# Optimization experiments

Hardware: AMD Instinct MI355X
Metric: run time of the kernel (lower is better)

## Reference

```python
import jax, jax.numpy as jnp
import numpy as np
import math

IN_DIM = 2048
OUT_DIM = 1152
SEQ_LEN = 8
WAY = 5
SHOT = 5
N_QUERIES = 100
MAX_LEN = int(SEQ_LEN * 1.5)
PE_SCALE = 0.1


def make_pe():
    pe = np.zeros((MAX_LEN, IN_DIM), dtype=np.float32)
    position = np.arange(0, MAX_LEN)[:, None].astype(np.float32)
    div_term = np.exp(np.arange(0, IN_DIM, 2).astype(np.float32) * -(math.log(10000.0) / IN_DIM))
    pe[:, 0::2] = np.sin(position * div_term) * PE_SCALE
    pe[:, 1::2] = np.cos(position * div_term) * PE_SCALE
    return jnp.asarray(pe)


def setup_inputs() -> dict:
    key = jax.random.key(0)
    ks = jax.random.split(key, 12)
    support_set = jax.random.normal(ks[0], (WAY * SHOT, SEQ_LEN, IN_DIM), dtype=jnp.float32)
    queries = jax.random.normal(ks[1], (N_QUERIES, SEQ_LEN, IN_DIM), dtype=jnp.float32)
    # labels: each class 0..WAY-1 appears SHOT times (sorted)
    support_labels = jnp.sort(jnp.arange(WAY * SHOT) % WAY)
    s = 1.0 / math.sqrt(IN_DIM)
    def lin(k):
        kw, kb = jax.random.split(k)
        W = jax.random.uniform(kw, (OUT_DIM, IN_DIM), minval=-s, maxval=s, dtype=jnp.float32)
        b = jax.random.uniform(kb, (OUT_DIM,), minval=-s, maxval=s, dtype=jnp.float32)
        return W, b
    sk_W, sk_b = lin(ks[2])
    sv_W, sv_b = lin(ks[3])
    qk_W, qk_b = lin(ks[4])
    qv_W, qv_b = lin(ks[5])
    return {
        "support_set": support_set,
        "support_labels": support_labels,
        "queries": queries,
        "sk_W": sk_W, "sk_b": sk_b,
        "sv_W": sv_W, "sv_b": sv_b,
        "qk_W": qk_W, "qk_b": qk_b,
        "qv_W": qv_W, "qv_b": qv_b,
        "ln_k_g": jnp.ones((OUT_DIM,), jnp.float32),
        "ln_k_b": jnp.zeros((OUT_DIM,), jnp.float32),
        "pe_table": make_pe(),
    }


def layer_norm(x, g, b, eps=1e-5):
    mu = jnp.mean(x, axis=-1, keepdims=True)
    var = jnp.var(x, axis=-1, keepdims=True)
    return (x - mu) / jnp.sqrt(var + eps) * g + b


def reference(support_set, support_labels, queries, sk_W, sk_b, sv_W, sv_b,
              qk_W, qk_b, qv_W, qv_b, ln_k_g, ln_k_b, pe_table):
    n_q, L, _ = queries.shape
    support_set = support_set + pe_table[None, :L]
    queries = queries + pe_table[None, :L]

    s_ks = layer_norm(support_set @ sk_W.T + sk_b, ln_k_g, ln_k_b)  # [S, L, D]
    q_ks = layer_norm(queries @ qk_W.T + qk_b, ln_k_g, ln_k_b)      # [Q, L, D]
    s_vs = support_set @ sv_W.T + sv_b                               # [S, L, D]
    q_vs = queries @ qv_W.T + qv_b                                   # [Q, L, D]

    D = q_ks.shape[-1]
    # group support by class: labels are sorted with equal shots per class
    k_bs = support_set.shape[0] // WAY
    class_k = s_ks.reshape(WAY, k_bs, L, D)   # [C, k, L, D]
    class_v = s_vs.reshape(WAY, k_bs, L, D)

    # scores: [C, Q, L(query), k*L(support)]
    scores = jnp.einsum('qld,ckmd->cqlkm', q_ks, class_k) / math.sqrt(D)
    scores = scores.reshape(WAY, n_q, L, k_bs * L)
    attn = jax.nn.softmax(scores, axis=-1)  # softmax over support frames per query frame
    attn = attn.reshape(WAY, n_q, L, k_bs, L).transpose(0, 1, 3, 2, 4)  # [C,Q,k,L,L]
    proto = jnp.einsum('cqklm,ckmd->cqld', attn, class_v)  # sum over k folded in

    diff = q_vs[None] - proto  # [C, Q, L, D]
    distance = jnp.sum(diff * diff, axis=(-2, -1)) / math.sqrt(D * L)  # [C, Q]
    return -distance.T  # [Q, C]
```

## Files before the change

kernel.cpp:

```cpp
#include <hip/hip_runtime.h>
#include <hip/hip_bf16.h>
#include <math.h>

#define WAY     5
#define NQ      100
#define SEQL    8
#define IN_DIM  2048
#define OUT_DIM 1152
#define QROWS   800
#define SROWS   200
#define QPAD    896
#define SPAD    256

#define OFF_SKB  0
#define OFF_SVB  1152
#define OFF_QKB  2304
#define OFF_QVB  3456
#define OFF_LNG  4608
#define OFF_LNB  5760
#define OFF_RSQ  6912
#define F32_END  7808

#define U_AQ   0
#define U_AS   (U_AQ  + QPAD*IN_DIM)
#define U_QKB  (U_AS  + SPAD*IN_DIM)
#define U_QVB  (U_QKB + QPAD*OUT_DIM)
#define U_SKB  (U_QVB + QPAD*OUT_DIM)
#define U_SVB  (U_SKB + SPAD*OUT_DIM)
#define PPSZ   (2304*OUT_DIM)
#define U_PP   (U_SVB + SPAD*OUT_DIM)
#define SPSZ   (2048*SPAD)
#define U_SP   (U_PP + 4*PPSZ)
#define U_W    (U_SP + 4*SPSZ)

typedef __attribute__((ext_vector_type(8))) short short8;
typedef __attribute__((ext_vector_type(4))) float f32x4;

__device__ __forceinline__ float bf2f(unsigned short u) {
    return __uint_as_float(((unsigned int)u) << 16);
}
__device__ __forceinline__ unsigned short f2bf(float f) {
    unsigned int u = __float_as_uint(f);
    return (unsigned short)((u + 0x7fffu + ((u >> 16) & 1u)) >> 16);
}
__device__ __forceinline__ bool sniff_bf16(const void* lng) {
    return *((const unsigned int*)lng) != 0x3F800000u;
}
__device__ __forceinline__ float load_s(const void* p, long idx, bool bf) {
    if (bf) return bf2f(((const unsigned short*)p)[idx]);
    return ((const float*)p)[idx];
}
__device__ __forceinline__ float4 load_v4(const void* p, long idx, bool bf) {
    if (bf) {
        ushort4 v = *((const ushort4*)((const unsigned short*)p + idx));
        return make_float4(bf2f(v.x), bf2f(v.y), bf2f(v.z), bf2f(v.w));
    }
    return *((const float4*)((const float*)p + idx));
}
__device__ __forceinline__ void gl_lds16(const unsigned short* g, unsigned short* l) {
    __builtin_amdgcn_global_load_lds(
        (const __attribute__((address_space(1))) unsigned int*)g,
        (__attribute__((address_space(3))) unsigned int*)l,
        16, 0, 0);
}

__global__ void stage_kernel(const void* support, const void* queries,
                             const void* skW, const void* svW,
                             const void* qkW, const void* qvW,
                             const void* skb, const void* svb,
                             const void* qkb, const void* qvb,
                             const void* lng, const void* lnb,
                             const void* pe, float* ws) {
    const bool bf = sniff_bf16(lng);
    unsigned short* ub = (unsigned short*)(ws + F32_END);
    const int tid = blockIdx.x * blockDim.x + threadIdx.x;
    const int stride = gridDim.x * blockDim.x;

    for (int i = tid; i < OUT_DIM; i += stride) {
        ws[OFF_SKB + i] = load_s(skb, i, bf);
        ws[OFF_SVB + i] = load_s(svb, i, bf);
        ws[OFF_QKB + i] = load_s(qkb, i, bf);
        ws[OFF_QVB + i] = load_s(qvb, i, bf);
        ws[OFF_LNG + i] = load_s(lng, i, bf);
        ws[OFF_LNB + i] = load_s(lnb, i, bf);
    }
    for (int i = tid; i < QPAD * (IN_DIM / 4); i += stride) {
        const int row = i >> 9, kc = (i & 511) * 4;
        ushort4 o;
        if (row < QROWS) {
            float4 v = load_v4(queries, (long)row * IN_DIM + kc, bf);
            const float4 p = load_v4(pe, (long)(row & 7) * IN_DIM + kc, bf);
            o.x = f2bf(v.x + p.x); o.y = f2bf(v.y + p.y);
            o.z = f2bf(v.z + p.z); o.w = f2bf(v.w + p.w);
        } else o = make_ushort4(0, 0, 0, 0);
        *(ushort4*)&ub[U_AQ + (long)row * IN_DIM + kc] = o;
    }
    for (int i = tid; i < SPAD * (IN_DIM / 4); i += stride) {
        const int row = i >> 9, kc = (i & 511) * 4;
        ushort4 o;
        if (row < SROWS) {
            float4 v = load_v4(support, (long)row * IN_DIM + kc, bf);
            const float4 p = load_v4(pe, (long)(row & 7) * IN_DIM + kc, bf);
            o.x = f2bf(v.x + p.x); o.y = f2bf(v.y + p.y);
            o.z = f2bf(v.z + p.z); o.w = f2bf(v.w + p.w);
        } else o = make_ushort4(0, 0, 0, 0);
        *(ushort4*)&ub[U_AS + (long)row * IN_DIM + kc] = o;
    }
    if (!bf) {
        const float* Wsrc[4] = {(const float*)qkW, (const float*)qvW,
                                (const float*)skW, (const float*)svW};
        for (int j = 0; j < 4; ++j) {
            unsigned short* dst = ub + U_W + (long)j * OUT_DIM * IN_DIM;
            const float* src = Wsrc[j];
            for (int i = tid; i < OUT_DIM * (IN_DIM / 4); i += stride) {
                const long e = (long)i * 4;
                const float4 v = *(const float4*)(src + e);
                ushort4 o;
                o.x = f2bf(v.x); o.y = f2bf(v.y); o.z = f2bf(v.z); o.w = f2bf(v.w);
                *(ushort4*)&dst[e] = o;
            }
        }
    }
}

__global__ __launch_bounds__(256) void proj_mfma(
        const void* skW, const void* svW, const void* qkW, const void* qvW,
        const void* lng, float* ws) {
    const bool is_bf = sniff_bf16(lng);
    unsigned short* ub = (unsigned short*)(ws + F32_END);
    const int job = blockIdx.z >> 2;
    const int chunk = blockIdx.z & 3;
    if (job >= 4) return;
    if (job >= 2 && blockIdx.y >= 2) return;

    const unsigned short* A = (job < 2) ? (ub + U_AQ) : (ub + U_AS);
    const unsigned short* W;
    if (is_bf) {
        const void* Wp[4] = {qkW, qvW, skW, svW};
        W = (const unsigned short*)Wp[job];
    } else {
        W = ub + U_W + (size_t)job * OUT_DIM * IN_DIM;
    }
    const int rowbase[4] = {0, 896, 1792, 2048};
    unsigned short* out = ub + U_PP + (size_t)chunk * PPSZ
                        + (size_t)rowbase[job] * OUT_DIM;

    const int r0 = blockIdx.y * 128;
    const int n0 = blockIdx.x * 128;
    const int kbeg = chunk * 512;

    __shared__ unsigned short Als[2][128 * 32];
    __shared__ unsigned short Bls[2][128 * 32];

    const int t = threadIdx.x, w = t >> 6, l = t & 63;
    const int wr = w >> 1, wc = w & 1;
    const int fm = l & 15, fq = l >> 4;
    const int srow = l >> 2, schunk = (l & 3) * 8;

    const unsigned short* Ag = A + (size_t)(r0 + w * 32 + srow) * IN_DIM + schunk + kbeg;
    const unsigned short* Bg = W + (size_t)(n0 + w * 32 + srow) * IN_DIM + schunk + kbeg;
    const int l0 = (w * 32) * 32;
    const int l1 = (w * 32 + 16) * 32;

    f32x4 acc[4][4] = {};

    gl_lds16(Ag, &Als[0][l0]);
    gl_lds16(Ag + (size_t)16 * IN_DIM, &Als[0][l1]);
    gl_lds16(Bg, &Bls[0][l0]);
    gl_lds16(Bg + (size_t)16 * IN_DIM, &Bls[0][l1]);
    __syncthreads();

    int cur = 0;
    for (int k0 = 0; k0 < 512; k0 += 32) {
        const int nxt = cur ^ 1;
        if (k0 + 32 < 512) {
            gl_lds16(Ag + k0 + 32, &Als[nxt][l0]);
            gl_lds16(Ag + (size_t)16 * IN_DIM + k0 + 32, &Als[nxt][l1]);
            gl_lds16(Bg + k0 + 32, &Bls[nxt][l0]);
            gl_lds16(Bg + (size_t)16 * IN_DIM + k0 + 32, &Bls[nxt][l1]);
        }

        short8 af[4], bff[4];
#pragma unroll
        for (int i = 0; i < 4; ++i)
            af[i] = *(const short8*)&Als[cur][(wr * 64 + i * 16 + fm) * 32 + fq * 8];
#pragma unroll
        for (int j = 0; j < 4; ++j)
            bff[j] = *(const short8*)&Bls[cur][(wc * 64 + j * 16 + fm) * 32 + fq * 8];
#pragma unroll
        for (int i = 0; i < 4; ++i)
#pragma unroll
            for (int j = 0; j < 4; ++j)
                acc[i][j] = __builtin_amdgcn_mfma_f32_16x16x32_bf16(
                    af[i], bff[j], acc[i][j], 0, 0, 0);

        __syncthreads();
        cur = nxt;
    }

#pragma unroll
    for (int j = 0; j < 4; ++j) {
        const int col = n0 + wc * 64 + j * 16 + fm;
#pragma unroll
        for (int i = 0; i < 4; ++i) {
            const int rb = r0 + wr * 64 + i * 16 + fq * 4;
            const f32x4 v = acc[i][j];
#pragma unroll
            for (int r = 0; r < 4; ++r)
                out[(size_t)(rb + r) * OUT_DIM + col] = f2bf(v[r]);
        }
    }
}

__global__ __launch_bounds__(256) void row_kernel(float* ws) {
    const int row = blockIdx.x;
    unsigned short* ub = (unsigned short*)(ws + F32_END);
    const unsigned short* pp = ub + U_PP + (size_t)row * OUT_DIM;
    const float* bias;
    unsigned short* outb;
    int mode, qrow = 0;
    if (row < 896)       { bias = ws + OFF_QKB; outb = ub + U_QKB + (size_t)row * OUT_DIM; mode = 0; }
    else if (row < 1792) { bias = ws + OFF_QVB; outb = ub + U_QVB + (size_t)(row - 896) * OUT_DIM; mode = 2; qrow = row - 896; }
    else if (row < 2048) { bias = ws + OFF_SKB; outb = ub + U_SKB + (size_t)(row - 1792) * OUT_DIM; mode = 0; }
    else                 { bias = ws + OFF_SVB; outb = ub + U_SVB + (size_t)(row - 2048) * OUT_DIM; mode = 1; }

    const int tid = threadIdx.x;
    __shared__ float red[8];
    __shared__ float xs[OUT_DIM];

    float s = 0.f, s2 = 0.f;
    for (int i = tid; i < OUT_DIM / 8; i += 256) {
        float v[8];
        {
            const float4 b0 = *(const float4*)(bias + i * 8);
            const float4 b1 = *(const float4*)(bias + i * 8 + 4);
            v[0] = b0.x; v[1] = b0.y; v[2] = b0.z; v[3] = b0.w;
            v[4] = b1.x; v[5] = b1.y; v[6] = b1.z; v[7] = b1.w;
        }
#pragma unroll
        for (int p = 0; p < 4; ++p) {
            const short8 u = *(const short8*)(pp + (size_t)p * PPSZ + i * 8);
#pragma unroll
            for (int k = 0; k < 8; ++k) v[k] += bf2f((unsigned short)u[k]);
        }
        if (mode == 0) {
#pragma unroll
            for (int k = 0; k < 8; ++k) {
                xs[i * 8 + k] = v[k];
                s += v[k];
                s2 = fmaf(v[k], v[k], s2);
            }
        } else {
#pragma unroll
            for (int k = 0; k < 8; ++k) {
                outb[i * 8 + k] = f2bf(v[k]);
                s2 = fmaf(v[k], v[k], s2);
            }
        }
    }

    if (mode == 0) {
        for (int o = 32; o > 0; o >>= 1) {
            s  += __shfl_down(s,  o, 64);
            s2 += __shfl_down(s2, o, 64);
        }
        if ((tid & 63) == 0) { red[tid >> 6] = s; red[4 + (tid >> 6)] = s2; }
        __syncthreads();
        const float S  = red[0] + red[1] + red[2] + red[3];
        const float S2 = red[4] + red[5] + red[6] + red[7];
        const float mu = S * (1.0f / OUT_DIM);
        const float var = S2 * (1.0f / OUT_DIM) - mu * mu;
        const float rs = rsqrtf(var + 1e-5f);
        const float* g = ws + OFF_LNG;
        const float* bn = ws + OFF_LNB;
        for (int i = tid; i < OUT_DIM; i += 256)
            outb[i] = f2bf((xs[i] - mu) * rs * g[i] + bn[i]);
    } else if (mode == 2) {
        for (int o = 32; o > 0; o >>= 1) s2 += __shfl_down(s2, o, 64);
        if ((tid & 63) == 0) red[tid >> 6] = s2;
        __syncthreads();
        if (tid == 0) ws[OFF_RSQ + qrow] = red[0] + red[1] + red[2] + red[3];
    }
}

__global__ __launch_bounds__(256) void pair_mfma(float* ws) {
    unsigned short* ub = (unsigned short*)(ws + F32_END);
    const int job = blockIdx.z >> 2;
    const int chunk = blockIdx.z & 3;
    if (job >= 3) return;
    if (job == 2 && blockIdx.y >= 4) return;

    const unsigned short* A;
    const unsigned short* B;
    int rowbase;
    if (job == 0)      { A = ub + U_QKB; B = ub + U_SKB; rowbase = 0; }
    else if (job == 1) { A = ub + U_QVB; B = ub + U_SVB; rowbase = 896; }
    else               { A = ub + U_SVB; B = ub + U_SVB; rowbase = 1792; }
    unsigned short* out = ub + U_SP + (size_t)chunk * SPSZ + (size_t)rowbase * SPAD;

    const int r0 = blockIdx.y * 64;
    const int n0 = blockIdx.x * 64;
    const int kbeg = chunk * 288;

    __shared__ unsigned short Als[2][64 * 32];
    __shared__ unsigned short Bls[2][64 * 32];

    const int t = threadIdx.x, w = t >> 6, l = t & 63;
    const int wr = w >> 1, wc = w & 1;
    const int fm = l & 15, fq = l >> 4;
    const int srow = l >> 2, schunk = (l & 3) * 8;

    const unsigned short* Ag = A + (size_t)(r0 + w * 16 + srow) * OUT_DIM + schunk + kbeg;
    const unsigned short* Bg = B + (size_t)(n0 + w * 16 + srow) * OUT_DIM + schunk + kbeg;
    const int lofs = (w * 16) * 32;

    f32x4 acc[2][2] = {};

    gl_lds16(Ag, &Als[0][lofs]);
    gl_lds16(Bg, &Bls[0][lofs]);
    __syncthreads();

    int cur = 0;
    for (int k0 = 0; k0 < 288; k0 += 32) {
        const int nxt = cur ^ 1;
        if (k0 + 32 < 288) {
            gl_lds16(Ag + k0 + 32, &Als[nxt][lofs]);
            gl_lds16(Bg + k0 + 32, &Bls[nxt][lofs]);
        }

        short8 af[2], bff[2];
#pragma unroll
        for (int i = 0; i < 2; ++i)
            af[i] = *(const short8*)&Als[cur][(wr * 32 + i * 16 + fm) * 32 + fq * 8];
#pragma unroll
        for (int j = 0; j < 2; ++j)
            bff[j] = *(const short8*)&Bls[cur][(wc * 32 + j * 16 + fm) * 32 + fq * 8];
#pragma unroll
        for (int i = 0; i < 2; ++i)
#pragma unroll
            for (int j = 0; j < 2; ++j)
                acc[i][j] = __builtin_amdgcn_mfma_f32_16x16x32_bf16(
                    af[i], bff[j], acc[i][j], 0, 0, 0);

        __syncthreads();
        cur = nxt;
    }

#pragma unroll
    for (int j = 0; j < 2; ++j) {
        const int col = n0 + wc * 32 + j * 16 + fm;
#pragma unroll
        for (int i = 0; i < 2; ++i) {
            const int rb = r0 + wr * 32 + i * 16 + fq * 4;
            const f32x4 v = acc[i][j];
#pragma unroll
            for (int r = 0; r < 4; ++r)
                out[(size_t)(rb + r) * SPAD + col] = f2bf(v[r]);
        }
    }
}

__global__ __launch_bounds__(256) void final_kernel(const void* lng, float* ws, void* outp) {
    const bool bf = sniff_bf16(lng);
    const int c = blockIdx.x;
    const int q = blockIdx.y;
    unsigned short* ub = (unsigned short*)(ws + F32_END);
    const unsigned short* P = ub + U_SP;

    __shared__ float sS[SEQL][40];
    __shared__ float sT[SEQL][40];
    __shared__ float sA[SEQL][40];
    __shared__ float sG[40][41];
    __shared__ float red[4];

    const int tid = threadIdx.x;
    const float isd = 0.029462782549439483f;

    for (int i = tid; i < SEQL * 40; i += 256) {
        const int l = i / 40, j = i % 40;
        const size_t rs = (size_t)(q * SEQL + l) * SPAD + c * 40 + j;
        const size_t rt = (size_t)(896 + q * SEQL + l) * SPAD + c * 40 + j;
        float s = 0.f, t = 0.f;
#pragma unroll
        for (int p = 0; p < 4; ++p) {
            s += bf2f(P[(size_t)p * SPSZ + rs]);
            t += bf2f(P[(size_t)p * SPSZ + rt]);
        }
        sS[l][j] = s * isd;
        sT[l][j] = t;
    }
    for (int i = tid; i < 40 * 40; i += 256) {
        const int j = i / 40, j2 = i % 40;
        const size_t rg = (size_t)(1792 + c * 40 + j) * SPAD + c * 40 + j2;
        float g = 0.f;
#pragma unroll
        for (int p = 0; p < 4; ++p) g += bf2f(P[(size_t)p * SPSZ + rg]);
        sG[j][j2] = g;
    }
    __syncthreads();

    if (tid < SEQL) {
        const int l = tid;
        float m = -1e30f;
        for (int j = 0; j < 40; ++j) m = fmaxf(m, sS[l][j]);
        float sum = 0.f;
        for (int j = 0; j < 40; ++j) { float e = __expf(sS[l][j] - m); sA[l][j] = e; sum += e; }
        const float inv = 1.0f / sum;
        for (int j = 0; j < 40; ++j) sA[l][j] *= inv;
    }
    __syncthreads();

    float part = 0.f;
    for (int i = tid; i < SEQL * 40; i += 256) {
        const int l = i / 40, j = i % 40;
        float gs = 0.f;
        for (int j2 = 0; j2 < 40; ++j2) gs = fmaf(sG[j][j2], sA[l][j2], gs);
        part += sA[l][j] * (gs - 2.0f * sT[l][j]);
    }
    for (int o = 32; o > 0; o >>= 1) part += __shfl_down(part, o, 64);
    if ((tid & 63) == 0) red[tid >> 6] = part;
    __syncthreads();

    if (tid == 0) {
        float qn = 0.f;
        for (int l = 0; l < SEQL; ++l) qn += ws[OFF_RSQ + q * SEQL + l];
        const float tot = red[0] + red[1] + red[2] + red[3] + qn;
        const float r = -(tot * (1.0f / 96.0f));
        if (bf) ((__hip_bfloat16*)outp)[q * WAY + c] = __float2bfloat16(r);
        else    ((float*)outp)[q * WAY + c] = r;
    }
}

extern "C" void kernel_launch(void* const* d_in, const int* in_sizes, int n_in,
                              void* d_out, int out_size, void* d_ws, size_t ws_size,
                              hipStream_t stream) {
    const void* support = d_in[0];
    const void* queries = d_in[2];
    const void* skW = d_in[3];  const void* skb = d_in[4];
    const void* svW = d_in[5];  const void* svb = d_in[6];
    const void* qkW = d_in[7];  const void* qkb = d_in[8];
    const void* qvW = d_in[9];  const void* qvb = d_in[10];
    const void* lng = d_in[11]; const void* lnb = d_in[12];
    const void* pe  = d_in[13];
    float* ws = (float*)d_ws;

    stage_kernel<<<dim3(512), dim3(256), 0, stream>>>(
        support, queries, skW, svW, qkW, qvW, skb, svb, qkb, qvb, lng, lnb, pe, ws);
    proj_mfma<<<dim3(9, 7, 16), dim3(256), 0, stream>>>(skW, svW, qkW, qvW, lng, ws);
    row_kernel<<<dim3(2304), dim3(256), 0, stream>>>(ws);
    pair_mfma<<<dim3(4, 14, 12), dim3(256), 0, stream>>>(ws);
    final_kernel<<<dim3(WAY, NQ), dim3(256), 0, stream>>>(lng, ws, d_out);
}
```

Before: 165.3 us.

## Drop split-K partials and weight staging; convert fp32 weights inside GEMM

```diff
diff --git a/kernel.cpp b/kernel.cpp
--- a/kernel.cpp
+++ b/kernel.cpp
@@ -27,11 +27,8 @@
 #define U_QVB  (U_QKB + QPAD*OUT_DIM)
 #define U_SKB  (U_QVB + QPAD*OUT_DIM)
 #define U_SVB  (U_SKB + SPAD*OUT_DIM)
-#define PPSZ   (2304*OUT_DIM)
-#define U_PP   (U_SVB + SPAD*OUT_DIM)
 #define SPSZ   (2048*SPAD)
-#define U_SP   (U_PP + 4*PPSZ)
-#define U_W    (U_SP + 4*SPSZ)
+#define U_SP   (U_SVB + SPAD*OUT_DIM)
 
 typedef __attribute__((ext_vector_type(8))) short short8;
 typedef __attribute__((ext_vector_type(4))) float f32x4;
@@ -63,10 +60,14 @@
         (__attribute__((address_space(3))) unsigned int*)l,
         16, 0, 0);
 }
+__device__ __forceinline__ void pack8(unsigned short* dst, float4 a, float4 b) {
+    union { unsigned short us[8]; short8 v; } u;
+    u.us[0] = f2bf(a.x); u.us[1] = f2bf(a.y); u.us[2] = f2bf(a.z); u.us[3] = f2bf(a.w);
+    u.us[4] = f2bf(b.x); u.us[5] = f2bf(b.y); u.us[6] = f2bf(b.z); u.us[7] = f2bf(b.w);
+    *(short8*)dst = u.v;
+}
 
 __global__ void stage_kernel(const void* support, const void* queries,
-                             const void* skW, const void* svW,
-                             const void* qkW, const void* qvW,
                              const void* skb, const void* svb,
                              const void* qkb, const void* qvb,
                              const void* lng, const void* lnb,
@@ -106,21 +107,6 @@
         } else o = make_ushort4(0, 0, 0, 0);
         *(ushort4*)&ub[U_AS + (long)row * IN_DIM + kc] = o;
     }
-    if (!bf) {
-        const float* Wsrc[4] = {(const float*)qkW, (const float*)qvW,
-                                (const float*)skW, (const float*)svW};
-        for (int j = 0; j < 4; ++j) {
-            unsigned short* dst = ub + U_W + (long)j * OUT_DIM * IN_DIM;
-            const float* src = Wsrc[j];
-            for (int i = tid; i < OUT_DIM * (IN_DIM / 4); i += stride) {
-                const long e = (long)i * 4;
-                const float4 v = *(const float4*)(src + e);
-                ushort4 o;
-                o.x = f2bf(v.x); o.y = f2bf(v.y); o.z = f2bf(v.z); o.w = f2bf(v.w);
-                *(ushort4*)&dst[e] = o;
-            }
-        }
-    }
 }
 
 __global__ __launch_bounds__(256) void proj_mfma(
@@ -128,144 +114,145 @@
         const void* lng, float* ws) {
     const bool is_bf = sniff_bf16(lng);
     unsigned short* ub = (unsigned short*)(ws + F32_END);
-    const int job = blockIdx.z >> 2;
-    const int chunk = blockIdx.z & 3;
-    if (job >= 4) return;
-    if (job >= 2 && blockIdx.y >= 2) return;
+
+    const int jj = (blockIdx.x & 7) * 81 + (blockIdx.x >> 3);
+
+    int job, nx, my;
+    if (jj < 504) { job = jj / 252; const int r = jj % 252; my = r % 14; nx = r / 14; }
+    else { const int t2 = jj - 504; job = 2 + t2 / 72; const int r = t2 % 72; my = r % 4; nx = r / 4; }
 
     const unsigned short* A = (job < 2) ? (ub + U_AQ) : (ub + U_AS);
-    const unsigned short* W;
-    if (is_bf) {
-        const void* Wp[4] = {qkW, qvW, skW, svW};
-        W = (const unsigned short*)Wp[job];
-    } else {
-        W = ub + U_W + (size_t)job * OUT_DIM * IN_DIM;
-    }
-    const int rowbase[4] = {0, 896, 1792, 2048};
-    unsigned short* out = ub + U_PP + (size_t)chunk * PPSZ
-                        + (size_t)rowbase[job] * OUT_DIM;
-
-    const int r0 = blockIdx.y * 128;
-    const int n0 = blockIdx.x * 128;
-    const int kbeg = chunk * 512;
-
-    __shared__ unsigned short Als[2][128 * 32];
-    __shared__ unsigned short Bls[2][128 * 32];
+    const void* Wv = (job == 0) ? qkW : (job == 1) ? qvW : (job == 2) ? skW : svW;
+    unsigned short* outb = (job == 0) ? ub + U_QKB : (job == 1) ? ub + U_QVB
+                         : (job == 2) ? ub + U_SKB : ub + U_SVB;
+    const float* bias = ws + ((job == 0) ? OFF_QKB : (job == 1) ? OFF_QVB
+                            : (job == 2) ? OFF_SKB : OFF_SVB);
+
+    const int r0 = my * 64, n0 = nx * 64;
+
+    __shared__ unsigned short Als[2][64 * 32];
+    __shared__ unsigned short Bls[2][64 * 32];
 
     const int t = threadIdx.x, w = t >> 6, l = t & 63;
     const int wr = w >> 1, wc = w & 1;
     const int fm = l & 15, fq = l >> 4;
     const int srow = l >> 2, schunk = (l & 3) * 8;
 
-    const unsigned short* Ag = A + (size_t)(r0 + w * 32 + srow) * IN_DIM + schunk + kbeg;
-    const unsigned short* Bg = W + (size_t)(n0 + w * 32 + srow) * IN_DIM + schunk + kbeg;
-    const int l0 = (w * 32) * 32;
-    const int l1 = (w * 32 + 16) * 32;
-
-    f32x4 acc[4][4] = {};
-
-    gl_lds16(Ag, &Als[0][l0]);
-    gl_lds16(Ag + (size_t)16 * IN_DIM, &Als[0][l1]);
-    gl_lds16(Bg, &Bls[0][l0]);
-    gl_lds16(Bg + (size_t)16 * IN_DIM, &Bls[0][l1]);
-    __syncthreads();
-
-    int cur = 0;
-    for (int k0 = 0; k0 < 512; k0 += 32) {
-        const int nxt = cur ^ 1;
-        if (k0 + 32 < 512) {
-            gl_lds16(Ag + k0 + 32, &Als[nxt][l0]);
-            gl_lds16(Ag + (size_t)16 * IN_DIM + k0 + 32, &Als[nxt][l1]);
-            gl_lds16(Bg + k0 + 32, &Bls[nxt][l0]);
-            gl_lds16(Bg + (size_t)16 * IN_DIM + k0 + 32, &Bls[nxt][l1]);
-        }
-
-        short8 af[4], bff[4];
-#pragma unroll
-        for (int i = 0; i < 4; ++i)
-            af[i] = *(const short8*)&Als[cur][(wr * 64 + i * 16 + fm) * 32 + fq * 8];
-#pragma unroll
-        for (int j = 0; j < 4; ++j)
-            bff[j] = *(const short8*)&Bls[cur][(wc * 64 + j * 16 + fm) * 32 + fq * 8];
-#pragma unroll
-        for (int i = 0; i < 4; ++i)
-#pragma unroll
-            for (int j = 0; j < 4; ++j)
-                acc[i][j] = __builtin_amdgcn_mfma_f32_16x16x32_bf16(
-                    af[i], bff[j], acc[i][j], 0, 0, 0);
-
+    const unsigned short* Ag = A + (size_t)(r0 + w * 16 + srow) * IN_DIM + schunk;
+    const int lofs = (w * 16) * 32;
+    const int d = lofs + l * 8;
+
+    f32x4 acc[2][2] = {};
+
+#define MFMA_CORE(BUF)                                                          \
+    {                                                                           \
+        short8 af[2], bff[2];                                                   \
+        _Pragma("unroll")                                                       \
+        for (int i = 0; i < 2; ++i)                                             \
+            af[i] = *(const short8*)&Als[BUF][(wr * 32 + i * 16 + fm) * 32 + fq * 8]; \
+        _Pragma("unroll")                                                       \
+        for (int j = 0; j < 2; ++j)                                             \
+            bff[j] = *(const short8*)&Bls[BUF][(wc * 32 + j * 16 + fm) * 32 + fq * 8]; \
+        _Pragma("unroll")                                                       \
+        for (int i = 0; i < 2; ++i)                                             \
+            _Pragma("unroll")                                                   \
+            for (int j = 0; j < 2; ++j)                                         \
+                acc[i][j] = __builtin_amdgcn_mfma_f32_16x16x32_bf16(            \
+                    af[i], bff[j], acc[i][j], 0, 0, 0);                         \
+    }
+
+    if (is_bf) {
+        const unsigned short* Bg = (const unsigned short*)Wv
+            + (size_t)(n0 + w * 16 + srow) * IN_DIM + schunk;
+        gl_lds16(Ag, &Als[0][lofs]);
+        gl_lds16(Bg, &Bls[0][lofs]);
         __syncthreads();
-        cur = nxt;
-    }
-
-#pragma unroll
-    for (int j = 0; j < 4; ++j) {
-        const int col = n0 + wc * 64 + j * 16 + fm;
-#pragma unroll
-        for (int i = 0; i < 4; ++i) {
-            const int rb = r0 + wr * 64 + i * 16 + fq * 4;
+        int cur = 0;
+        for (int k0 = 0; k0 < IN_DIM; k0 += 32) {
+            const int nxt = cur ^ 1;
+            if (k0 + 32 < IN_DIM) {
+                gl_lds16(Ag + k0 + 32, &Als[nxt][lofs]);
+                gl_lds16(Bg + k0 + 32, &Bls[nxt][lofs]);
+            }
+            MFMA_CORE(cur)
+            __syncthreads();
+            cur = nxt;
+        }
+    } else {
+        const float* Bgf = (const float*)Wv
+            + (size_t)(n0 + w * 16 + srow) * IN_DIM + schunk;
+        {
+            const float4 x0 = *(const float4*)(Bgf);
+            const float4 x1 = *(const float4*)(Bgf + 4);
+            pack8(&Bls[0][d], x0, x1);
+            gl_lds16(Ag, &Als[0][lofs]);
+            __syncthreads();
+        }
+        int cur = 0;
+        for (int k0 = 0; k0 < IN_DIM; k0 += 32) {
+            const int nxt = cur ^ 1;
+            float4 x0, x1;
+            const bool more = (k0 + 32 < IN_DIM);
+            if (more) {
+                x0 = *(const float4*)(Bgf + k0 + 32);
+                x1 = *(const float4*)(Bgf + k0 + 36);
+                gl_lds16(Ag + k0 + 32, &Als[nxt][lofs]);
+            }
+            MFMA_CORE(cur)
+            if (more) pack8(&Bls[nxt][d], x0, x1);
+            __syncthreads();
+            cur = nxt;
+        }
+    }
+#undef MFMA_CORE
+
+#pragma unroll
+    for (int j = 0; j < 2; ++j) {
+        const int col = n0 + wc * 32 + j * 16 + fm;
+        const float bv = bias[col];
+#pragma unroll
+        for (int i = 0; i < 2; ++i) {
+            const int rb = r0 + wr * 32 + i * 16 + fq * 4;
             const f32x4 v = acc[i][j];
 #pragma unroll
             for (int r = 0; r < 4; ++r)
-                out[(size_t)(rb + r) * OUT_DIM + col] = f2bf(v[r]);
-        }
-    }
-}
-
-__global__ __launch_bounds__(256) void row_kernel(float* ws) {
+                outb[(size_t)(rb + r) * OUT_DIM + col] = f2bf(v[r] + bv);
+        }
+    }
+}
+
+__global__ __launch_bounds__(256) void finish_kernel(float* ws) {
     const int row = blockIdx.x;
     unsigned short* ub = (unsigned short*)(ws + F32_END);
-    const unsigned short* pp = ub + U_PP + (size_t)row * OUT_DIM;
-    const float* bias;
-    unsigned short* outb;
+    const int tid = threadIdx.x;
+    __shared__ float xs[OUT_DIM];
+    __shared__ float red[8];
+
+    unsigned short* rp;
     int mode, qrow = 0;
-    if (row < 896)       { bias = ws + OFF_QKB; outb = ub + U_QKB + (size_t)row * OUT_DIM; mode = 0; }
-    else if (row < 1792) { bias = ws + OFF_QVB; outb = ub + U_QVB + (size_t)(row - 896) * OUT_DIM; mode = 2; qrow = row - 896; }
-    else if (row < 2048) { bias = ws + OFF_SKB; outb = ub + U_SKB + (size_t)(row - 1792) * OUT_DIM; mode = 0; }
-    else                 { bias = ws + OFF_SVB; outb = ub + U_SVB + (size_t)(row - 2048) * OUT_DIM; mode = 1; }
-
-    const int tid = threadIdx.x;
-    __shared__ float red[8];
-    __shared__ float xs[OUT_DIM];
+    if (row < 896)       { rp = ub + U_QKB + (size_t)row * OUT_DIM; mode = 0; }
+    else if (row < 1152) { rp = ub + U_SKB + (size_t)(row - 896) * OUT_DIM; mode = 0; }
+    else                 { rp = ub + U_QVB + (size_t)(row - 1152) * OUT_DIM; mode = 1; qrow = row - 1152; }
 
     float s = 0.f, s2 = 0.f;
     for (int i = tid; i < OUT_DIM / 8; i += 256) {
-        float v[8];
-        {
-            const float4 b0 = *(const float4*)(bias + i * 8);
-            const float4 b1 = *(const float4*)(bias + i * 8 + 4);
-            v[0] = b0.x; v[1] = b0.y; v[2] = b0.z; v[3] = b0.w;
-            v[4] = b1.x; v[5] = b1.y; v[6] = b1.z; v[7] = b1.w;
-        }
-#pragma unroll
-        for (int p = 0; p < 4; ++p) {
-            const short8 u = *(const short8*)(pp + (size_t)p * PPSZ + i * 8);
-#pragma unroll
-            for (int k = 0; k < 8; ++k) v[k] += bf2f((unsigned short)u[k]);
-        }
-        if (mode == 0) {
-#pragma unroll
-            for (int k = 0; k < 8; ++k) {
-                xs[i * 8 + k] = v[k];
-                s += v[k];
-                s2 = fmaf(v[k], v[k], s2);
-            }
-        } else {
-#pragma unroll
-            for (int k = 0; k < 8; ++k) {
-                outb[i * 8 + k] = f2bf(v[k]);
-                s2 = fmaf(v[k], v[k], s2);
-            }
-        }
-    }
+        const short8 u = *(const short8*)(rp + i * 8);
+#pragma unroll
+        for (int k = 0; k < 8; ++k) {
+            const float v = bf2f((unsigned short)u[k]);
+            s += v;
+            s2 = fmaf(v, v, s2);
+            if (mode == 0) xs[i * 8 + k] = v;
+        }
+    }
+    for (int o = 32; o > 0; o >>= 1) {
+        s  += __shfl_down(s,  o, 64);
+        s2 += __shfl_down(s2, o, 64);
+    }
+    if ((tid & 63) == 0) { red[tid >> 6] = s; red[4 + (tid >> 6)] = s2; }
+    __syncthreads();
 
     if (mode == 0) {
-        for (int o = 32; o > 0; o >>= 1) {
-            s  += __shfl_down(s,  o, 64);
-            s2 += __shfl_down(s2, o, 64);
-        }
-        if ((tid & 63) == 0) { red[tid >> 6] = s; red[4 + (tid >> 6)] = s2; }
-        __syncthreads();
         const float S  = red[0] + red[1] + red[2] + red[3];
         const float S2 = red[4] + red[5] + red[6] + red[7];
         const float mu = S * (1.0f / OUT_DIM);
@@ -274,12 +261,9 @@
         const float* g = ws + OFF_LNG;
         const float* bn = ws + OFF_LNB;
         for (int i = tid; i < OUT_DIM; i += 256)
-            outb[i] = f2bf((xs[i] - mu) * rs * g[i] + bn[i]);
-    } else if (mode == 2) {
-        for (int o = 32; o > 0; o >>= 1) s2 += __shfl_down(s2, o, 64);
-        if ((tid & 63) == 0) red[tid >> 6] = s2;
-        __syncthreads();
-        if (tid == 0) ws[OFF_RSQ + qrow] = red[0] + red[1] + red[2] + red[3];
+            rp[i] = f2bf((xs[i] - mu) * rs * g[i] + bn[i]);
+    } else if (tid == 0) {
+        ws[OFF_RSQ + qrow] = red[4] + red[5] + red[6] + red[7];
     }
 }
 
@@ -445,9 +429,9 @@
     float* ws = (float*)d_ws;
 
     stage_kernel<<<dim3(512), dim3(256), 0, stream>>>(
-        support, queries, skW, svW, qkW, qvW, skb, svb, qkb, qvb, lng, lnb, pe, ws);
-    proj_mfma<<<dim3(9, 7, 16), dim3(256), 0, stream>>>(skW, svW, qkW, qvW, lng, ws);
-    row_kernel<<<dim3(2304), dim3(256), 0, stream>>>(ws);
+        support, queries, skb, svb, qkb, qvb, lng, lnb, pe, ws);
+    proj_mfma<<<dim3(648), dim3(256), 0, stream>>>(skW, svW, qkW, qvW, lng, ws);
+    finish_kernel<<<dim3(2048), dim3(256), 0, stream>>>(ws);
     pair_mfma<<<dim3(4, 14, 12), dim3(256), 0, stream>>>(ws);
     final_kernel<<<dim3(WAY, NQ), dim3(256), 0, stream>>>(lng, ws, d_out);
 }
```

Measured after the change: 180.0 us. 1.09x slower.
